# Optimization experiments

Measured on AMD Instinct MI355X. Metric: run time of the kernel, lower is better.

Reference implementation:

```python
import jax, jax.numpy as jnp
import numpy as np
import math

B, S, D = 8, 4096, 64

def setup_inputs() -> dict:
    key = jax.random.key(0)
    k1, k2, k3 = jax.random.split(key, 3)
    value = jax.random.normal(k1, (B, S, D), dtype=jnp.float32)
    key_t = jax.random.normal(k2, (B, S, D), dtype=jnp.float32)
    query = jax.random.normal(k3, (B, S, D), dtype=jnp.float32)
    return {"value": value, "key": key_t, "query": query}

def reference(value, key, query):
    # scores[b, q, k] = sum_d query[b,q,d] * key[b,k,d]
    scores = jnp.einsum('bqd,bkd->bqk', query, key) / math.sqrt(query.shape[-1])
    # NOTE: softmax over dim=1 (the QUERY axis), matching the original torch code
    attn = jax.nn.softmax(scores, axis=1)
    # outputs[b, q, d] = sum_k attn[b,q,k] * value[b,k,d]
    return jnp.einsum('bqk,bkd->bqd', attn, value)
```

## Files before the change

kernel.cpp:

```cpp
#include <hip/hip_runtime.h>

#define Bn 8
#define Sn 4096
#define Dn 64

constexpr int NKT = Sn / 64;
constexpr int NQT = Sn / 128;

typedef _Float16 half_t;
typedef __attribute__((ext_vector_type(2))) _Float16 half2v;
typedef __attribute__((ext_vector_type(4))) _Float16 half4;
typedef __attribute__((ext_vector_type(8))) _Float16 half8;
typedef __attribute__((ext_vector_type(4))) float f32x4;

constexpr float SCALE = 0.125f;
constexpr float SCALE2 = 0.125f * 1.4426950408889634f;

#define MFMA32(a, b, c) __builtin_amdgcn_mfma_f32_16x16x32_f16((a), (b), (c), 0, 0, 0)
#define MFMA16(a, b, c) __builtin_amdgcn_mfma_f32_16x16x16f16((a), (b), (c), 0, 0, 0)

__device__ __forceinline__ float fexp2(float x) {
#if defined(__has_builtin) && __has_builtin(__builtin_amdgcn_exp2f)
  return __builtin_amdgcn_exp2f(x);
#else
  return exp2f(x);
#endif
}

__device__ __forceinline__ int swz_k(int row, int col) {
  return row * 64 + (col ^ ((row & 7) << 3));
}
__device__ __forceinline__ int swz_v(int row, int col) {
  return row * 64 + (col ^ (((row & 7) << 3) ^ (((row >> 3) & 7) << 2)));
}

__device__ __forceinline__ void cvt8(const float* s, half8& h, half8& l) {
  #pragma unroll
  for (int j = 0; j < 8; ++j) {
    half_t hh = (half_t)s[j];
    h[j] = hh;
    l[j] = (half_t)(s[j] - (float)hh);
  }
}

__device__ __forceinline__ void cp16(half_t* lds, const half_t* g) {
  __builtin_amdgcn_global_load_lds(
      (const __attribute__((address_space(1))) unsigned int*)g,
      (__attribute__((address_space(3))) unsigned int*)lds, 16, 0, 0);
}


__global__ __launch_bounds__(256, 2)
void prep_q(const float* __restrict__ Qg, half_t* __restrict__ QhW,
            half_t* __restrict__ QlW) {
  const int t = threadIdx.x;
  const int b = blockIdx.x & 7, qt = blockIdx.x >> 3;
  const float* Qb = Qg + ((size_t)(b * Sn + qt * 128)) * Dn;
  half_t* qh = QhW + ((size_t)(b * NQT + qt)) * 8192;
  half_t* ql = QlW + ((size_t)(b * NQT + qt)) * 8192;
  #pragma unroll
  for (int i = 0; i < 8; ++i) {
    int f = t + 256 * i, q = f >> 4, d4 = (f & 15) << 2;
    float4 v = *(const float4*)(Qb + (size_t)q * Dn + d4);
    float s4[4] = {v.x * SCALE2, v.y * SCALE2, v.z * SCALE2, v.w * SCALE2};
    half4 h, l;
    #pragma unroll
    for (int j = 0; j < 4; ++j) {
      half_t hh = (half_t)s4[j];
      h[j] = hh;
      l[j] = (half_t)(s4[j] - (float)hh);
    }
    *(half4*)&qh[swz_k(q, d4)] = h;
    *(half4*)&ql[swz_k(q, d4)] = l;
  }
}

__global__ __launch_bounds__(256, 2)
void attn_linv(const float* __restrict__ Kg, const float* __restrict__ Vg,
               const half_t* __restrict__ QhW, const half_t* __restrict__ QlW,
               float* __restrict__ lg2inv, half_t* __restrict__ KVW) {
  __shared__ alignas(16) half_t Qh_s[2][8192];
  __shared__ alignas(16) half_t Ql_s[2][8192];
  __shared__ alignas(16) float red[4][4][16];

  const int t = threadIdx.x;
  const int lane = t & 63, w = t >> 6, g = lane >> 4, c16 = lane & 15;
  const int b = blockIdx.x & 7, kx = blockIdx.x >> 3;
  const int k0 = kx * 64;

  half_t* blob = KVW + ((size_t)(b * NKT + kx)) * 8192;

  half8 kfh[4][2];
  #pragma unroll
  for (int ks = 0; ks < 4; ++ks)
    #pragma unroll
    for (int c = 0; c < 2; ++c) {
      const float* src = Kg + ((size_t)(b * Sn + k0 + 16 * ks + c16)) * Dn + 32 * c + 8 * g;
      float a8[8];
      *(float4*)&a8[0] = *(const float4*)src;
      *(float4*)&a8[4] = *(const float4*)(src + 4);
      #pragma unroll
      for (int j = 0; j < 8; ++j) kfh[ks][c][j] = (half_t)a8[j];
    }
  {
    #pragma unroll
    for (int ks = 0; ks < 4; ++ks)
      if (ks == w) {
        #pragma unroll
        for (int c = 0; c < 2; ++c)
          *(half8*)&blob[swz_k(16 * ks + c16, 32 * c + 8 * g)] = kfh[ks][c];
      }
  }
  {
    const float* Vb = Vg + ((size_t)(b * Sn + k0)) * Dn;
    #pragma unroll
    for (int i = 0; i < 2; ++i) {
      int u = t + 256 * i;
      int k2 = u >> 4, dg = u & 15;
      float4 v0 = *(const float4*)(Vb + (size_t)(2 * k2) * Dn + 4 * dg);
      float4 v1 = *(const float4*)(Vb + (size_t)(2 * k2 + 1) * Dn + 4 * dg);
      const float* v0p = (const float*)&v0;
      const float* v1p = (const float*)&v1;
      #pragma unroll
      for (int j = 0; j < 4; ++j) {
        half2v pair = {(half_t)v0p[j], (half_t)v1p[j]};
        *(half2v*)&blob[4096 + swz_v(4 * dg + j, 2 * k2)] = pair;
      }
    }
  }

  const half_t* qhw = QhW + (size_t)b * NQT * 8192;
  const half_t* qlw = QlW + (size_t)b * NQT * 8192;

  auto load_q = [&](int bb, int qt) {
    const size_t toff = (size_t)qt * 8192;
    #pragma unroll
    for (int c = 0; c < 4; ++c) {
      const int ch = (c * 4 + w) * 512;
      cp16(&Qh_s[bb][ch], qhw + toff + ch + lane * 8);
      cp16(&Ql_s[bb][ch], qlw + toff + ch + lane * 8);
    }
  };

  float lsum[4] = {0.f, 0.f, 0.f, 0.f};

  load_q(0, 0);
  __syncthreads();
  for (int qt = 0; qt < NQT; ++qt) {
    if (qt + 1 < NQT) load_q((qt + 1) & 1, qt + 1);
    const int cur = qt & 1;
    #pragma unroll
    for (int qs = 0; qs < 2; ++qs) {
      const int qloc = 32 * w + 16 * qs + c16;
      half8 qh[2], ql[2];
      #pragma unroll
      for (int c = 0; c < 2; ++c) {
        qh[c] = *(const half8*)&Qh_s[cur][swz_k(qloc, 32 * c + 8 * g)];
        ql[c] = *(const half8*)&Ql_s[cur][swz_k(qloc, 32 * c + 8 * g)];
      }
      #pragma unroll
      for (int ks = 0; ks < 4; ++ks) {
        f32x4 acc = {0.f, 0.f, 0.f, 0.f};
        acc = MFMA32(qh[0], kfh[ks][0], acc);
        acc = MFMA32(qh[1], kfh[ks][1], acc);
        acc = MFMA32(ql[0], kfh[ks][0], acc);
        acc = MFMA32(ql[1], kfh[ks][1], acc);
        lsum[ks] += fexp2(acc[0]) + fexp2(acc[1]) + fexp2(acc[2]) + fexp2(acc[3]);
      }
    }
    __syncthreads();
  }

  #pragma unroll
  for (int ks = 0; ks < 4; ++ks) {
    lsum[ks] += __shfl_xor(lsum[ks], 16);
    lsum[ks] += __shfl_xor(lsum[ks], 32);
  }
  __syncthreads();
  if (lane < 16) {
    #pragma unroll
    for (int ks = 0; ks < 4; ++ks) red[w][ks][lane] = lsum[ks];
  }
  __syncthreads();
  if (t < 64) {
    int ks = t >> 4, c = t & 15;
    float tot = red[0][ks][c] + red[1][ks][c] + red[2][ks][c] + red[3][ks][c];
    lg2inv[(size_t)b * Sn + k0 + 16 * ks + c] = -log2f(tot);
  }
}

__global__ __launch_bounds__(512, 4)
void attn_pv(const half_t* __restrict__ KVW, const float* __restrict__ Qg,
             const float* __restrict__ lg2inv, float* __restrict__ Og) {
  __shared__ alignas(16) half_t KV_s[2][8192];

  const int t = threadIdx.x;
  const int lane = t & 63, w = t >> 6;
  const int g = (lane >> 4) & 3, c16 = lane & 15;
  const int wk = w & 3, wq = w >> 2;
  const int b = blockIdx.x & 7;
  const int q0 = (blockIdx.x >> 3) * 64;

  half8 qh[2][2], ql[2][2];
  #pragma unroll
  for (int qs = 0; qs < 2; ++qs) {
    const int qrow = q0 + 32 * wq + 16 * qs + c16;
    #pragma unroll
    for (int c = 0; c < 2; ++c) {
      const float* src = Qg + ((size_t)(b * Sn + qrow)) * Dn + 32 * c + 8 * g;
      float a8[8];
      *(float4*)&a8[0] = *(const float4*)src;
      *(float4*)&a8[4] = *(const float4*)(src + 4);
      #pragma unroll
      for (int j = 0; j < 8; ++j) a8[j] *= SCALE2;
      cvt8(a8, qh[qs][c], ql[qs][c]);
    }
  }

  f32x4 accO[2][4];
  #pragma unroll
  for (int qs = 0; qs < 2; ++qs)
    #pragma unroll
    for (int ds = 0; ds < 4; ++ds) accO[qs][ds] = {0.f, 0.f, 0.f, 0.f};

  auto load_kv = [&](int bb, int kt) {
    const half_t* src = KVW + ((size_t)(b * NKT + kt)) * 8192;
    half_t* dst = KV_s[bb];
    cp16(dst + w * 512, src + w * 512 + lane * 8);
    cp16(dst + 4096 + w * 512, src + 4096 + w * 512 + lane * 8);
  };

  const int krow = 16 * wk + c16;
  const int okh0 = swz_k(krow, 8 * g);
  const int okh1 = swz_k(krow, 32 + 8 * g);
  const float* lgp = lg2inv + (size_t)b * Sn + 16 * wk + 4 * g;

  load_kv(0, 0);
  __syncthreads();
  for (int kt = 0; kt < NKT; ++kt) {
    if (kt + 1 < NKT) load_kv((kt + 1) & 1, kt + 1);
    const int cur = kt & 1;
    const half_t* KH = &KV_s[cur][0];
    const half_t* VT = &KV_s[cur][4096];

    half8 kh0 = *(const half8*)&KH[okh0];
    half8 kh1 = *(const half8*)&KH[okh1];
    f32x4 lg4 = *(const f32x4*)(lgp + (size_t)kt * 64);

    f32x4 sv[2];
    __builtin_amdgcn_s_setprio(1);
    #pragma unroll
    for (int qs = 0; qs < 2; ++qs) {
      f32x4 acc = lg4;
      acc = MFMA32(kh0, qh[qs][0], acc);
      acc = MFMA32(kh1, qh[qs][1], acc);
      acc = MFMA32(kh0, ql[qs][0], acc);
      acc = MFMA32(kh1, ql[qs][1], acc);
      sv[qs] = acc;
    }
    __builtin_amdgcn_s_setprio(0);

    half4 ph[2];
    #pragma unroll
    for (int qs = 0; qs < 2; ++qs) {
      float p0 = fexp2(sv[qs][0]);
      float p1 = fexp2(sv[qs][1]);
      float p2 = fexp2(sv[qs][2]);
      float p3 = fexp2(sv[qs][3]);
      ph[qs] = {(half_t)p0, (half_t)p1, (half_t)p2, (half_t)p3};
    }

    __builtin_amdgcn_s_setprio(1);
    #pragma unroll
    for (int ds = 0; ds < 4; ++ds) {
      half4 vt = *(const half4*)&VT[swz_v(16 * ds + c16, 16 * wk + 4 * g)];
      accO[0][ds] = MFMA16(vt, ph[0], accO[0][ds]);
      accO[1][ds] = MFMA16(vt, ph[1], accO[1][ds]);
    }
    __builtin_amdgcn_s_setprio(0);

    __syncthreads();
  }

  float* red = (float*)&KV_s[0][0];
  #pragma unroll
  for (int qs = 0; qs < 2; ++qs) {
    if (wk != 0) {
      #pragma unroll
      for (int ds = 0; ds < 4; ++ds)
        *(f32x4*)&red[(((wq * 3 + (wk - 1)) * 4) + ds) * 256 + lane * 4] = accO[qs][ds];
    }
    __syncthreads();
    if (wk == 0) {
      const int qrow = q0 + 32 * wq + 16 * qs + c16;
      float* Ob = Og + ((size_t)(b * Sn + qrow)) * Dn;
      #pragma unroll
      for (int ds = 0; ds < 4; ++ds) {
        f32x4 o = accO[qs][ds];
        #pragma unroll
        for (int j = 0; j < 3; ++j)
          o += *(const f32x4*)&red[(((wq * 3 + j) * 4) + ds) * 256 + lane * 4];
        *(f32x4*)(Ob + 16 * ds + 4 * g) = o;
      }
    }
    __syncthreads();
  }
}

__global__ __launch_bounds__(256, 2)
void fb_attn_linv(const float* __restrict__ Kg, const float* __restrict__ Qg,
                  float* __restrict__ linv) {
  __shared__ alignas(16) half_t Qh_s[128 * 64];
  __shared__ alignas(16) half_t Ql_s[128 * 64];
  __shared__ alignas(16) float red[4][4][16];

  const int t = threadIdx.x;
  const int lane = t & 63, w = t >> 6, g = lane >> 4, c16 = lane & 15;
  const int b = blockIdx.y;
  const int k0 = blockIdx.x * 64;

  half8 kfh[4][2], kfl[4][2];
  #pragma unroll
  for (int ks = 0; ks < 4; ++ks)
    #pragma unroll
    for (int c = 0; c < 2; ++c) {
      const float* src = Kg + ((size_t)(b * Sn + k0 + 16 * ks + c16)) * Dn + 32 * c + 8 * g;
      float a8[8];
      *(float4*)&a8[0] = *(const float4*)src;
      *(float4*)&a8[4] = *(const float4*)(src + 4);
      cvt8(a8, kfh[ks][c], kfl[ks][c]);
    }

  float lsum[4] = {0.f, 0.f, 0.f, 0.f};

  for (int q0 = 0; q0 < Sn; q0 += 128) {
    __syncthreads();
    const float* Qb = Qg + ((size_t)(b * Sn + q0)) * Dn;
    #pragma unroll
    for (int i = 0; i < 8; ++i) {
      int f = t + 256 * i, q = f >> 4, d4 = (f & 15) << 2;
      float4 v = *(const float4*)(Qb + (size_t)q * Dn + d4);
      float s4[4] = {v.x * SCALE, v.y * SCALE, v.z * SCALE, v.w * SCALE};
      half4 h, l;
      #pragma unroll
      for (int j = 0; j < 4; ++j) {
        half_t hh = (half_t)s4[j];
        h[j] = hh;
        l[j] = (half_t)(s4[j] - (float)hh);
      }
      *(half4*)&Qh_s[swz_k(q, d4)] = h;
      *(half4*)&Ql_s[swz_k(q, d4)] = l;
    }
    __syncthreads();

    #pragma unroll
    for (int qs = 0; qs < 2; ++qs) {
      const int qloc = 32 * w + 16 * qs + c16;
      half8 qh[2], ql[2];
      #pragma unroll
      for (int c = 0; c < 2; ++c) {
        qh[c] = *(const half8*)&Qh_s[swz_k(qloc, 32 * c + 8 * g)];
        ql[c] = *(const half8*)&Ql_s[swz_k(qloc, 32 * c + 8 * g)];
      }
      #pragma unroll
      for (int ks = 0; ks < 4; ++ks) {
        f32x4 acc = {0.f, 0.f, 0.f, 0.f};
        acc = MFMA32(qh[0], kfh[ks][0], acc);
        acc = MFMA32(qh[1], kfh[ks][1], acc);
        acc = MFMA32(ql[0], kfh[ks][0], acc);
        acc = MFMA32(ql[1], kfh[ks][1], acc);
        acc = MFMA32(qh[0], kfl[ks][0], acc);
        acc = MFMA32(qh[1], kfl[ks][1], acc);
        lsum[ks] += __expf(acc[0]) + __expf(acc[1]) + __expf(acc[2]) + __expf(acc[3]);
      }
    }
  }

  #pragma unroll
  for (int ks = 0; ks < 4; ++ks) {
    lsum[ks] += __shfl_xor(lsum[ks], 16);
    lsum[ks] += __shfl_xor(lsum[ks], 32);
  }
  __syncthreads();
  if (lane < 16) {
    #pragma unroll
    for (int ks = 0; ks < 4; ++ks) red[w][ks][lane] = lsum[ks];
  }
  __syncthreads();
  if (t < 64) {
    int ks = t >> 4, c = t & 15;
    float tot = red[0][ks][c] + red[1][ks][c] + red[2][ks][c] + red[3][ks][c];
    linv[(size_t)b * Sn + k0 + 16 * ks + c] = 1.0f / tot;
  }
}

__global__ __launch_bounds__(512, 2)
void fb_attn_pv(const float* __restrict__ Vg, const float* __restrict__ Kg,
                const float* __restrict__ Qg, const float* __restrict__ linv,
                float* __restrict__ Og) {
  __shared__ alignas(16) half_t Kh_s[64 * 64];
  __shared__ alignas(16) half_t Kl_s[64 * 64];
  __shared__ alignas(16) half_t Vt_s[64 * 64];
  __shared__ alignas(16) float li_s[64];
  __shared__ alignas(16) float red[4][2][4][256];

  const int t = threadIdx.x;
  const int lane = t & 63, w = t >> 6;
  const int g = (lane >> 4) & 3, c16 = lane & 15;
  const int wq = w & 3, wk = w >> 2;
  const int b = blockIdx.y;
  const int q0 = blockIdx.x * 128;

  half8 qh[2][2], ql[2][2];
  #pragma unroll
  for (int qs = 0; qs < 2; ++qs) {
    const int qrow = q0 + 32 * wq + 16 * qs + c16;
    #pragma unroll
    for (int c = 0; c < 2; ++c) {
      const float* src = Qg + ((size_t)(b * Sn + qrow)) * Dn + 32 * c + 8 * g;
      float a8[8];
      *(float4*)&a8[0] = *(const float4*)src;
      *(float4*)&a8[4] = *(const float4*)(src + 4);
      #pragma unroll
      for (int j = 0; j < 8; ++j) a8[j] *= SCALE;
      cvt8(a8, qh[qs][c], ql[qs][c]);
    }
  }

  f32x4 accO[2][4];
  #pragma unroll
  for (int qs = 0; qs < 2; ++qs)
    #pragma unroll
    for (int ds = 0; ds < 4; ++ds) accO[qs][ds] = {0.f, 0.f, 0.f, 0.f};

  const int krow0 = t >> 4, kd40 = (t & 15) << 2;
  const int krow1 = 32 + (t >> 4), kd41 = kd40;
  const int vk2 = t >> 4, vdg = t & 15;

  float4 kreg0, kreg1, vreg0, vreg1;
  float li_reg = 0.f;
  {
    const float* Kb = Kg + ((size_t)(b * Sn)) * Dn;
    const float* Vb = Vg + ((size_t)(b * Sn)) * Dn;
    kreg0 = *(const float4*)(Kb + (size_t)krow0 * Dn + kd40);
    kreg1 = *(const float4*)(Kb + (size_t)krow1 * Dn + kd41);
    vreg0 = *(const float4*)(Vb + (size_t)(2 * vk2) * Dn + 4 * vdg);
    vreg1 = *(const float4*)(Vb + (size_t)(2 * vk2 + 1) * Dn + 4 * vdg);
    if (t < 64) li_reg = linv[(size_t)b * Sn + t];
  }

  for (int kt = 0; kt < Sn / 64; ++kt) {
    __syncthreads();
    {
      const float* k0p = (const float*)&kreg0;
      const float* k1p = (const float*)&kreg1;
      half4 h, l;
      #pragma unroll
      for (int j = 0; j < 4; ++j) {
        half_t hh = (half_t)k0p[j];
        h[j] = hh; l[j] = (half_t)(k0p[j] - (float)hh);
      }
      *(half4*)&Kh_s[swz_k(krow0, kd40)] = h;
      *(half4*)&Kl_s[swz_k(krow0, kd40)] = l;
      #pragma unroll
      for (int j = 0; j < 4; ++j) {
        half_t hh = (half_t)k1p[j];
        h[j] = hh; l[j] = (half_t)(k1p[j] - (float)hh);
      }
      *(half4*)&Kh_s[swz_k(krow1, kd41)] = h;
      *(half4*)&Kl_s[swz_k(krow1, kd41)] = l;

      const float* v0p = (const float*)&vreg0;
      const float* v1p = (const float*)&vreg1;
      #pragma unroll
      for (int j = 0; j < 4; ++j) {
        half2v pair = {(half_t)v0p[j], (half_t)v1p[j]};
        *(half2v*)&Vt_s[swz_v(4 * vdg + j, 2 * vk2)] = pair;
      }
      if (t < 64) li_s[t] = li_reg;
    }
    __syncthreads();

    if (kt + 1 < Sn / 64) {
      const float* Kb = Kg + ((size_t)(b * Sn + (kt + 1) * 64)) * Dn;
      const float* Vb = Vg + ((size_t)(b * Sn + (kt + 1) * 64)) * Dn;
      kreg0 = *(const float4*)(Kb + (size_t)krow0 * Dn + kd40);
      kreg1 = *(const float4*)(Kb + (size_t)krow1 * Dn + kd41);
      vreg0 = *(const float4*)(Vb + (size_t)(2 * vk2) * Dn + 4 * vdg);
      vreg1 = *(const float4*)(Vb + (size_t)(2 * vk2 + 1) * Dn + 4 * vdg);
      if (t < 64) li_reg = linv[(size_t)b * Sn + (kt + 1) * 64 + t];
    }

    #pragma unroll
    for (int kss = 0; kss < 2; ++kss) {
      const int ks = 2 * wk + kss;
      const int krow = 16 * ks + c16;
      half8 kh0 = *(const half8*)&Kh_s[swz_k(krow, 8 * g)];
      half8 kh1 = *(const half8*)&Kh_s[swz_k(krow, 32 + 8 * g)];
      half8 kl0 = *(const half8*)&Kl_s[swz_k(krow, 8 * g)];
      half8 kl1 = *(const half8*)&Kl_s[swz_k(krow, 32 + 8 * g)];
      f32x4 li4 = *(const f32x4*)&li_s[16 * ks + 4 * g];

      half4 ph[2];
      #pragma unroll
      for (int qs = 0; qs < 2; ++qs) {
        f32x4 acc = {0.f, 0.f, 0.f, 0.f};
        acc = MFMA32(kh0, qh[qs][0], acc);
        acc = MFMA32(kh1, qh[qs][1], acc);
        acc = MFMA32(kh0, ql[qs][0], acc);
        acc = MFMA32(kh1, ql[qs][1], acc);
        acc = MFMA32(kl0, qh[qs][0], acc);
        acc = MFMA32(kl1, qh[qs][1], acc);
        float p0 = __expf(acc[0]) * li4[0];
        float p1 = __expf(acc[1]) * li4[1];
        float p2 = __expf(acc[2]) * li4[2];
        float p3 = __expf(acc[3]) * li4[3];
        ph[qs] = {(half_t)p0, (half_t)p1, (half_t)p2, (half_t)p3};
      }
      #pragma unroll
      for (int ds = 0; ds < 4; ++ds) {
        half4 vt = *(const half4*)&Vt_s[swz_v(16 * ds + c16, 16 * ks + 4 * g)];
        accO[0][ds] = MFMA16(vt, ph[0], accO[0][ds]);
        accO[1][ds] = MFMA16(vt, ph[1], accO[1][ds]);
      }
    }
  }

  if (wk == 1) {
    #pragma unroll
    for (int qs = 0; qs < 2; ++qs)
      #pragma unroll
      for (int ds = 0; ds < 4; ++ds)
        *(f32x4*)&red[wq][qs][ds][lane * 4] = accO[qs][ds];
  }
  __syncthreads();
  if (wk == 0) {
    #pragma unroll
    for (int qs = 0; qs < 2; ++qs) {
      const int qrow = q0 + 32 * wq + 16 * qs + c16;
      float* Ob = Og + ((size_t)(b * Sn + qrow)) * Dn;
      #pragma unroll
      for (int ds = 0; ds < 4; ++ds) {
        f32x4 o = accO[qs][ds] + *(const f32x4*)&red[wq][qs][ds][lane * 4];
        *(f32x4*)(Ob + 16 * ds + 4 * g) = o;
      }
    }
  }
}

extern "C" void kernel_launch(void* const* d_in, const int* in_sizes, int n_in,
                              void* d_out, int out_size, void* d_ws, size_t ws_size,
                              hipStream_t stream) {
  const float* V = reinterpret_cast<const float*>(d_in[0]);
  const float* K = reinterpret_cast<const float*>(d_in[1]);
  const float* Q = reinterpret_cast<const float*>(d_in[2]);
  float* O = reinterpret_cast<float*>(d_out);

  char* ws = reinterpret_cast<char*>(d_ws);
  const size_t MB = 1024 * 1024;
  const size_t WS_NEEDED = 21 * MB;

  float* li = reinterpret_cast<float*>(ws);
  if (ws_size >= WS_NEEDED) {
    half_t* QhW = reinterpret_cast<half_t*>(ws + 1 * MB);
    half_t* QlW = reinterpret_cast<half_t*>(ws + 5 * MB);
    half_t* KVW = reinterpret_cast<half_t*>(ws + 9 * MB);
    prep_q<<<dim3(NQT * Bn), dim3(256), 0, stream>>>(Q, QhW, QlW);
    attn_linv<<<dim3(NKT * Bn), dim3(256), 0, stream>>>(K, V, QhW, QlW, li, KVW);
    attn_pv<<<dim3((Sn / 64) * Bn), dim3(512), 0, stream>>>(KVW, Q, li, O);
  } else {
    fb_attn_linv<<<dim3(Sn / 64, Bn), dim3(256), 0, stream>>>(K, Q, li);
    fb_attn_pv<<<dim3(Sn / 128, Bn), dim3(512), 0, stream>>>(V, K, Q, li, O);
  }
}
```

Measured before the change: 108.6 us.

## Halve query tile per block in PV kernel to raise occupancy

```diff
diff --git a/kernel.cpp b/kernel.cpp
--- a/kernel.cpp
+++ b/kernel.cpp
@@ -189,7 +189,7 @@
   }
 }
 
-__global__ __launch_bounds__(512, 4)
+__global__ __launch_bounds__(512, 8)
 void attn_pv(const half_t* __restrict__ KVW, const float* __restrict__ Qg,
              const float* __restrict__ lg2inv, float* __restrict__ Og) {
   __shared__ alignas(16) half_t KV_s[2][8192];
@@ -199,29 +199,24 @@
   const int g = (lane >> 4) & 3, c16 = lane & 15;
   const int wk = w & 3, wq = w >> 2;
   const int b = blockIdx.x & 7;
-  const int q0 = (blockIdx.x >> 3) * 64;
-
-  half8 qh[2][2], ql[2][2];
-  #pragma unroll
-  for (int qs = 0; qs < 2; ++qs) {
-    const int qrow = q0 + 32 * wq + 16 * qs + c16;
-    #pragma unroll
-    for (int c = 0; c < 2; ++c) {
-      const float* src = Qg + ((size_t)(b * Sn + qrow)) * Dn + 32 * c + 8 * g;
-      float a8[8];
-      *(float4*)&a8[0] = *(const float4*)src;
-      *(float4*)&a8[4] = *(const float4*)(src + 4);
-      #pragma unroll
-      for (int j = 0; j < 8; ++j) a8[j] *= SCALE2;
-      cvt8(a8, qh[qs][c], ql[qs][c]);
-    }
-  }
-
-  f32x4 accO[2][4];
-  #pragma unroll
-  for (int qs = 0; qs < 2; ++qs)
-    #pragma unroll
-    for (int ds = 0; ds < 4; ++ds) accO[qs][ds] = {0.f, 0.f, 0.f, 0.f};
+  const int q0 = (blockIdx.x >> 3) * 32;
+  const int qrow = q0 + 16 * wq + c16;
+
+  half8 qh[2], ql[2];
+  #pragma unroll
+  for (int c = 0; c < 2; ++c) {
+    const float* src = Qg + ((size_t)(b * Sn + qrow)) * Dn + 32 * c + 8 * g;
+    float a8[8];
+    *(float4*)&a8[0] = *(const float4*)src;
+    *(float4*)&a8[4] = *(const float4*)(src + 4);
+    #pragma unroll
+    for (int j = 0; j < 8; ++j) a8[j] *= SCALE2;
+    cvt8(a8, qh[c], ql[c]);
+  }
+
+  f32x4 accO[4];
+  #pragma unroll
+  for (int ds = 0; ds < 4; ++ds) accO[ds] = {0.f, 0.f, 0.f, 0.f};
 
   auto load_kv = [&](int bb, int kt) {
     const half_t* src = KVW + ((size_t)(b * NKT + kt)) * 8192;
@@ -247,35 +242,22 @@
     half8 kh1 = *(const half8*)&KH[okh1];
     f32x4 lg4 = *(const f32x4*)(lgp + (size_t)kt * 64);
 
-    f32x4 sv[2];
     __builtin_amdgcn_s_setprio(1);
-    #pragma unroll
-    for (int qs = 0; qs < 2; ++qs) {
-      f32x4 acc = lg4;
-      acc = MFMA32(kh0, qh[qs][0], acc);
-      acc = MFMA32(kh1, qh[qs][1], acc);
-      acc = MFMA32(kh0, ql[qs][0], acc);
-      acc = MFMA32(kh1, ql[qs][1], acc);
-      sv[qs] = acc;
-    }
+    f32x4 acc = lg4;
+    acc = MFMA32(kh0, qh[0], acc);
+    acc = MFMA32(kh1, qh[1], acc);
+    acc = MFMA32(kh0, ql[0], acc);
+    acc = MFMA32(kh1, ql[1], acc);
     __builtin_amdgcn_s_setprio(0);
 
-    half4 ph[2];
-    #pragma unroll
-    for (int qs = 0; qs < 2; ++qs) {
-      float p0 = fexp2(sv[qs][0]);
-      float p1 = fexp2(sv[qs][1]);
-      float p2 = fexp2(sv[qs][2]);
-      float p3 = fexp2(sv[qs][3]);
-      ph[qs] = {(half_t)p0, (half_t)p1, (half_t)p2, (half_t)p3};
-    }
+    half4 ph = {(half_t)fexp2(acc[0]), (half_t)fexp2(acc[1]),
+                (half_t)fexp2(acc[2]), (half_t)fexp2(acc[3])};
 
     __builtin_amdgcn_s_setprio(1);
     #pragma unroll
     for (int ds = 0; ds < 4; ++ds) {
       half4 vt = *(const half4*)&VT[swz_v(16 * ds + c16, 16 * wk + 4 * g)];
-      accO[0][ds] = MFMA16(vt, ph[0], accO[0][ds]);
-      accO[1][ds] = MFMA16(vt, ph[1], accO[1][ds]);
+      accO[ds] = MFMA16(vt, ph, accO[ds]);
     }
     __builtin_amdgcn_s_setprio(0);
 
@@ -283,27 +265,22 @@
   }
 
   float* red = (float*)&KV_s[0][0];
-  #pragma unroll
-  for (int qs = 0; qs < 2; ++qs) {
-    if (wk != 0) {
-      #pragma unroll
-      for (int ds = 0; ds < 4; ++ds)
-        *(f32x4*)&red[(((wq * 3 + (wk - 1)) * 4) + ds) * 256 + lane * 4] = accO[qs][ds];
-    }
-    __syncthreads();
-    if (wk == 0) {
-      const int qrow = q0 + 32 * wq + 16 * qs + c16;
-      float* Ob = Og + ((size_t)(b * Sn + qrow)) * Dn;
-      #pragma unroll
-      for (int ds = 0; ds < 4; ++ds) {
-        f32x4 o = accO[qs][ds];
-        #pragma unroll
-        for (int j = 0; j < 3; ++j)
-          o += *(const f32x4*)&red[(((wq * 3 + j) * 4) + ds) * 256 + lane * 4];
-        *(f32x4*)(Ob + 16 * ds + 4 * g) = o;
-      }
-    }
-    __syncthreads();
+  if (wk != 0) {
+    #pragma unroll
+    for (int ds = 0; ds < 4; ++ds)
+      *(f32x4*)&red[(((wq * 3 + (wk - 1)) * 4) + ds) * 256 + lane * 4] = accO[ds];
+  }
+  __syncthreads();
+  if (wk == 0) {
+    float* Ob = Og + ((size_t)(b * Sn + qrow)) * Dn;
+    #pragma unroll
+    for (int ds = 0; ds < 4; ++ds) {
+      f32x4 o = accO[ds];
+      #pragma unroll
+      for (int j = 0; j < 3; ++j)
+        o += *(const f32x4*)&red[(((wq * 3 + j) * 4) + ds) * 256 + lane * 4];
+      *(f32x4*)(Ob + 16 * ds + 4 * g) = o;
+    }
   }
 }
 
@@ -567,7 +544,7 @@
     half_t* KVW = reinterpret_cast<half_t*>(ws + 9 * MB);
     prep_q<<<dim3(NQT * Bn), dim3(256), 0, stream>>>(Q, QhW, QlW);
     attn_linv<<<dim3(NKT * Bn), dim3(256), 0, stream>>>(K, V, QhW, QlW, li, KVW);
-    attn_pv<<<dim3((Sn / 64) * Bn), dim3(512), 0, stream>>>(KVW, Q, li, O);
+    attn_pv<<<dim3((Sn / 32) * Bn), dim3(512), 0, stream>>>(KVW, Q, li, O);
   } else {
     fb_attn_linv<<<dim3(Sn / 64, Bn), dim3(256), 0, stream>>>(K, Q, li);
     fb_attn_pv<<<dim3(Sn / 128, Bn), dim3(512), 0, stream>>>(V, K, Q, li, O);
```

Result: slower. 128.6 us (+18.4%).
